# Kernel tuning notes

Measured on AMD Instinct MI355X. Metric: run time of the kernel, lower is better.

The kernel has to match this reference:

```python
import jax, jax.numpy as jnp
import numpy as np

# dims
B, N, T, D = 32, 207, 12, 128
H, HD, L, FF = 8, 16, 4, 512
PL, OD, IN = 12, 1, 1
SCALE = 1.0 / float(np.sqrt(HD))
NEG = -1e9


def ln(x, g, b, eps=1e-5):
    m = jnp.mean(x, -1, keepdims=True)
    v = jnp.mean((x - m) ** 2, -1, keepdims=True)
    return (x - m) * jax.lax.rsqrt(v + eps) * g + b


def setup_inputs() -> dict:
    key = jax.random.key(0)
    keys = iter(jax.random.split(key, 48))
    def rn(shape, s=0.02):
        return jax.random.normal(next(keys), shape, jnp.float32) * s
    z = lambda *s: jnp.zeros(s, jnp.float32)
    o = lambda *s: jnp.ones(s, jnp.float32)
    inp = {
        "x": jax.random.normal(next(keys), (B, N, T, IN), jnp.float32),
        "adj": jax.random.randint(next(keys), (N, N), 0, 2, jnp.int32),
        "Wi": rn((IN, D)), "bi": z(D),
        # spatial blocks (stacked over L layers)
        "Wq": rn((L, D, D)), "Wk": rn((L, D, D)), "Wv": rn((L, D, D)),
        "Wo": rn((L, D, D)), "bo": z(L, D),
        "sW1": rn((L, D, FF)), "sB1": z(L, FF), "sW2": rn((L, FF, D)), "sB2": z(L, D),
        "sg1": o(L, D), "sh1": z(L, D), "sg2": o(L, D), "sh2": z(L, D),
        # temporal blocks
        "Win": rn((L, D, 3 * D)), "Bin": z(L, 3 * D), "Wout": rn((L, D, D)), "Bout": z(L, D),
        "tW1": rn((L, D, FF)), "tB1": z(L, FF), "tW2": rn((L, FF, D)), "tB2": z(L, D),
        "tg1": o(L, D), "th1": z(L, D), "tg2": o(L, D), "th2": z(L, D),
        # prediction head
        "P1": rn((D, 2 * D)), "Pb1": z(2 * D), "P2": rn((2 * D, D)), "Pb2": z(D),
        "P3": rn((D, PL * OD)), "Pb3": z(PL * OD),
    }
    return inp


def reference(x, adj, Wi, bi, Wq, Wk, Wv, Wo, bo, sW1, sB1, sW2, sB2,
              sg1, sh1, sg2, sh2, Win, Bin, Wout, Bout, tW1, tB1, tW2, tB2,
              tg1, th1, tg2, th2, P1, Pb1, P2, Pb2, P3, Pb3):
    mask = (adj == 0)  # [N,N] True = masked (no edge)
    cmask = jnp.triu(jnp.ones((T, T), bool), 1)  # causal mask over time
    h = x @ Wi + bi  # [B,N,T,D]
    for l in range(L):
        # --- spatial adjacency-masked attention (vectorized over t) ---
        xn = ln(h, sg1[l], sh1[l])
        q = (xn @ Wq[l]).reshape(B, N, T, H, HD)
        k = (xn @ Wk[l]).reshape(B, N, T, H, HD)
        v = (xn @ Wv[l]).reshape(B, N, T, H, HD)
        sc = jnp.einsum('bnthd,bmthd->bthnm', q, k) * SCALE  # [B,T,H,N,N]
        sc = jnp.where(mask[None, None, None], NEG, sc)
        a = jax.nn.softmax(sc, -1)
        o = jnp.einsum('bthnm,bmthd->bnthd', a, v).reshape(B, N, T, D)
        h = h + o @ Wo[l] + bo[l]
        xn = ln(h, sg2[l], sh2[l])
        h = h + jax.nn.relu(xn @ sW1[l] + sB1[l]) @ sW2[l] + sB2[l]
        # --- temporal causal attention (per node) ---
        xn = ln(h, tg1[l], th1[l])
        qkv = xn @ Win[l] + Bin[l]
        q, k, v = jnp.split(qkv, 3, -1)
        q = q.reshape(B, N, T, H, HD)
        k = k.reshape(B, N, T, H, HD)
        v = v.reshape(B, N, T, H, HD)
        sc = jnp.einsum('bnthd,bnshd->bnhts', q, k) * SCALE  # [B,N,H,T,T]
        sc = jnp.where(cmask[None, None, None], NEG, sc)
        a = jax.nn.softmax(sc, -1)
        o = jnp.einsum('bnhts,bnshd->bnthd', a, v).reshape(B, N, T, D)
        h = h + o @ Wout[l] + Bout[l]
        xn = ln(h, tg2[l], th2[l])
        h = h + jax.nn.relu(xn @ tW1[l] + tB1[l]) @ tW2[l] + tB2[l]
    # prediction head on last time step
    hl = h[:, :, -1, :]  # [B,N,D]
    zz = jax.nn.relu(hl @ P1 + Pb1)
    zz = jax.nn.relu(zz @ P2 + Pb2)
    return (zz @ P3 + Pb3).reshape(B, N, PL, OD)
```

## Files before the change

### kernel.cpp

```cpp
#include <hip/hip_runtime.h>
#include <hip/hip_bf16.h>

#define B_   32
#define N_   207
#define T_   12
#define D_   128
#define H_   8
#define HD_  16
#define L_   4
#define FF_  512
#define PL_  12
#define TOK  (B_*N_*T_)
#define ROWS2 (B_*N_)
#define SCALE_ 0.25f
#define NEG_  -1e9f
#define NPAD 208
#define KQ2  24
#define KVH  232
#define SLAB 3312

typedef __hip_bfloat16 bf16;
typedef unsigned int u32;
typedef __attribute__((ext_vector_type(8))) short bf16x8;
typedef __attribute__((ext_vector_type(8))) _Float16 f16x8;
typedef __attribute__((ext_vector_type(4))) float f32x4;

__device__ __forceinline__ float b2f(bf16 x){ return __bfloat162float(x); }
__device__ __forceinline__ bf16  f2b(float x){ return __float2bfloat16(x); }

__device__ __forceinline__ void gll16(const bf16* g, bf16* l){
  __builtin_amdgcn_global_load_lds((const __attribute__((address_space(1))) void*)g,
                                   (__attribute__((address_space(3))) void*)l, 16, 0, 0);
}

__global__ void detect_k(const void* x, int* flag){
  __shared__ int cnt[256];
  const unsigned short* u = (const unsigned short*)x;
  int ok = 0;
  for (int i = threadIdx.x; i < 4096; i += 256){
    unsigned int bits = ((unsigned int)u[i]) << 16;
    float f = __uint_as_float(bits);
    float a = fabsf(f);
    if (f == 0.0f || (a > 1e-4f && a < 64.0f)) ok++;
  }
  cnt[threadIdx.x] = ok;
  __syncthreads();
  for (int s = 128; s > 0; s >>= 1){
    if (threadIdx.x < s) cnt[threadIdx.x] += cnt[threadIdx.x + s];
    __syncthreads();
  }
  if (threadIdx.x == 0) *flag = (cnt[0] > 3686) ? 1 : 0;
}

struct FlatArgs {
  const void* src[24];
  long long dst[24];
  int cum[25];
};
__global__ void cvt_flat_k(FlatArgs a, bf16* base, const int* flag, int total){
  int i = blockIdx.x*256 + threadIdx.x;
  if (i >= total) return;
  int j = 0;
  while (i >= a.cum[j+1]) j++;
  int loc = i - a.cum[j];
  float v = (*flag) ? b2f(((const bf16*)a.src[j])[loc]) : ((const float*)a.src[j])[loc];
  base[a.dst[j] + loc] = f2b(v);
}

struct TArgs {
  const void* src[10];
  long long dst[10];
  int K[10], Nc[10], Lstr[10], ro[10];
  float scale[10];
  int cum[11];
};
__global__ void cvt_t_k(TArgs a, bf16* base, const int* flag, int total){
  int i = blockIdx.x*256 + threadIdx.x;
  if (i >= total) return;
  int j = 0;
  while (i >= a.cum[j+1]) j++;
  int loc = i - a.cum[j];
  int KN = a.K[j]*a.Nc[j];
  int l = loc / KN; int rm = loc - l*KN; int k = rm / a.Nc[j]; int n = rm - k*a.Nc[j];
  float v = (*flag) ? b2f(((const bf16*)a.src[j])[loc]) : ((const float*)a.src[j])[loc];
  base[a.dst[j] + (long long)l*a.Lstr[j] + (long long)(a.ro[j]+n)*a.K[j] + k] = f2b(v*a.scale[j]);
}

__global__ void abits_k(const int* adj, u32* out){
  int i = blockIdx.x*256 + threadIdx.x;
  if (i >= NPAD*7) return;
  int n = i / 7, wj = i % 7;
  u32 v = 0;
  if (n < N_){
    for (int bit = 0; bit < 32; bit++){
      int m = wj*32 + bit;
      if (m < N_ && adj[n*N_ + m] != 0) v |= (1u << bit);
    }
  }
  out[i] = v;
}

__global__ void embed_ln_k(const bf16* x, const bf16* Wi, const bf16* bi,
                           const bf16* g, const bf16* bta, float* h, bf16* xnb){
  int wave = threadIdx.x >> 6, lane = threadIdx.x & 63;
  int tok = blockIdx.x*4 + wave;
  if (tok >= TOK) return;
  float xv = b2f(x[tok]);
  float v0 = xv*b2f(Wi[lane])    + b2f(bi[lane]);
  float v1 = xv*b2f(Wi[lane+64]) + b2f(bi[lane+64]);
  float* hp = h + (size_t)tok*D_;
  hp[lane] = v0; hp[lane+64] = v1;
  float s = v0 + v1;
  for (int off = 32; off >= 1; off >>= 1) s += __shfl_xor(s, off, 64);
  float m = s * (1.0f/128.0f);
  float d0 = v0 - m, d1 = v1 - m;
  float vv = d0*d0 + d1*d1;
  for (int off = 32; off >= 1; off >>= 1) vv += __shfl_xor(vv, off, 64);
  float r = rsqrtf(vv*(1.0f/128.0f) + 1e-5f);
  bf16* op = xnb + (size_t)tok*D_;
  op[lane]    = f2b(d0*r*b2f(g[lane])    + b2f(bta[lane]));
  op[lane+64] = f2b(d1*r*b2f(g[lane+64]) + b2f(bta[lane+64]));
}

__global__ __launch_bounds__(256) void mgemm_k(const bf16* __restrict__ A,
    const bf16* __restrict__ Wt, const bf16* __restrict__ bias,
    bf16* __restrict__ outp, int ldo, int Ktot, int relu){
  __shared__ __align__(16) bf16 As[128*32];
  __shared__ __align__(16) bf16 Bs[128*32];
  int tid = threadIdx.x;
  int rowBase = blockIdx.y * 128, colBase = blockIdx.x * 128;
  int w = tid >> 6, lane = tid & 63, quad = lane >> 4, cl = lane & 15;
  int waveM = w >> 1, waveN = w & 1;
  f32x4 accr[4][4];
  #pragma unroll
  for (int i = 0; i < 4; i++)
    #pragma unroll
    for (int j = 0; j < 4; j++) accr[i][j] = (f32x4){0.f,0.f,0.f,0.f};
  int lr = tid >> 2, kc = tid & 3;
  const bf16* Ap = A  + (size_t)(rowBase + lr)*Ktot + kc*8;
  const bf16* Bp = Wt + (size_t)(colBase + lr)*Ktot + kc*8;
  bf16* AsW = As + tid*8;
  bf16* BsW = Bs + tid*8;
  for (int kk = 0; kk < Ktot; kk += 32){
    __syncthreads();
    gll16(Ap + kk, AsW);
    gll16(Ap + (size_t)64*Ktot + kk, AsW + 64*32);
    gll16(Bp + kk, BsW);
    gll16(Bp + (size_t)64*Ktot + kk, BsW + 64*32);
    __syncthreads();
    bf16x8 af[4], bfr[4];
    #pragma unroll
    for (int mi = 0; mi < 4; mi++)
      af[mi] = *(const bf16x8*)(As + (waveM*64 + mi*16 + cl)*32 + quad*8);
    #pragma unroll
    for (int nj = 0; nj < 4; nj++)
      bfr[nj] = *(const bf16x8*)(Bs + (waveN*64 + nj*16 + cl)*32 + quad*8);
    #pragma unroll
    for (int mi = 0; mi < 4; mi++)
      #pragma unroll
      for (int nj = 0; nj < 4; nj++)
        accr[mi][nj] = __builtin_amdgcn_mfma_f32_16x16x32_bf16(af[mi], bfr[nj], accr[mi][nj], 0,0,0);
  }
  float bv[4];
  #pragma unroll
  for (int nj = 0; nj < 4; nj++)
    bv[nj] = bias ? b2f(bias[colBase + waveN*64 + nj*16 + cl]) : 0.0f;
  #pragma unroll
  for (int mi = 0; mi < 4; mi++){
    int row0 = rowBase + waveM*64 + mi*16 + quad*4;
    #pragma unroll
    for (int nj = 0; nj < 4; nj++){
      int col = colBase + waveN*64 + nj*16 + cl;
      #pragma unroll
      for (int r = 0; r < 4; r++){
        float v = accr[mi][nj][r] + bv[nj];
        if (relu) v = fmaxf(v, 0.0f);
        outp[(size_t)(row0+r)*ldo + col] = f2b(v);
      }
    }
  }
}

__global__ __launch_bounds__(256) void mgemm_qkvT_k(const bf16* __restrict__ A,
    const bf16* __restrict__ Wt, bf16* __restrict__ sQ,
    bf16* __restrict__ sK, bf16* __restrict__ sV){
  __shared__ __align__(16) bf16 As[128*32];
  __shared__ __align__(16) bf16 Bs[128*32];
  const int Ktot = 128;
  int tid = threadIdx.x;
  int rowBase = blockIdx.y * 128, colBase = blockIdx.x * 128;
  int w = tid >> 6, lane = tid & 63, quad = lane >> 4, cl = lane & 15;
  int waveM = w >> 1, waveN = w & 1;
  f32x4 accr[4][4];
  #pragma unroll
  for (int i = 0; i < 4; i++)
    #pragma unroll
    for (int j = 0; j < 4; j++) accr[i][j] = (f32x4){0.f,0.f,0.f,0.f};
  int lr = tid >> 2, kc = tid & 3;
  const bf16* Ap = A  + (size_t)(rowBase + lr)*Ktot + kc*8;
  const bf16* Bp = Wt + (size_t)(colBase + lr)*Ktot + kc*8;
  bf16* AsW = As + tid*8;
  bf16* BsW = Bs + tid*8;
  for (int kk = 0; kk < Ktot; kk += 32){
    __syncthreads();
    gll16(Ap + kk, AsW);
    gll16(Ap + (size_t)64*Ktot + kk, AsW + 64*32);
    gll16(Bp + kk, BsW);
    gll16(Bp + (size_t)64*Ktot + kk, BsW + 64*32);
    __syncthreads();
    bf16x8 af[4], bfr[4];
    #pragma unroll
    for (int mi = 0; mi < 4; mi++)
      af[mi] = *(const bf16x8*)(As + (waveM*64 + mi*16 + cl)*32 + quad*8);
    #pragma unroll
    for (int nj = 0; nj < 4; nj++)
      bfr[nj] = *(const bf16x8*)(Bs + (waveN*64 + nj*16 + cl)*32 + quad*8);
    #pragma unroll
    for (int mi = 0; mi < 4; mi++)
      #pragma unroll
      for (int nj = 0; nj < 4; nj++)
        accr[mi][nj] = __builtin_amdgcn_mfma_f32_16x16x32_bf16(af[mi], bfr[nj], accr[mi][nj], 0,0,0);
  }
  #pragma unroll
  for (int mi = 0; mi < 4; mi++){
    #pragma unroll
    for (int r = 0; r < 4; r++){
      int tok = rowBase + waveM*64 + mi*16 + quad*4 + r;
      int bn = tok / T_; int t = tok - bn*T_;
      int b = bn / N_;  int n = bn - b*N_;
      size_t base = ((size_t)(b*T_ + t)*H_)*SLAB + n*16 + cl;
      #pragma unroll
      for (int nj = 0; nj < 4; nj++){
        int col = colBase + waveN*64 + nj*16;
        int part = col >> 7, hh = (col >> 4) & 7;
        bf16* dst = (part == 0) ? sQ : (part == 1) ? sK : sV;
        dst[base + (size_t)hh*SLAB] = f2b(accr[mi][nj][r]);
      }
    }
  }
}

__global__ __launch_bounds__(256) void mgemm_ln_k(const bf16* __restrict__ A,
    const bf16* __restrict__ Wt, const bf16* __restrict__ bias,
    float* __restrict__ hout, int Ktot,
    const bf16* __restrict__ g, const bf16* __restrict__ bta,
    bf16* __restrict__ xnb){
  __shared__ __align__(16) bf16 As[128*32];
  __shared__ __align__(16) bf16 Bs[128*32];
  __shared__ float red[2][128][2];
  int tid = threadIdx.x;
  int rowBase = blockIdx.y * 128;
  int w = tid >> 6, lane = tid & 63, quad = lane >> 4, cl = lane & 15;
  int waveM = w >> 1, waveN = w & 1;
  f32x4 accr[4][4];
  #pragma unroll
  for (int i = 0; i < 4; i++)
    #pragma unroll
    for (int j = 0; j < 4; j++) accr[i][j] = (f32x4){0.f,0.f,0.f,0.f};
  int lr = tid >> 2, kc = tid & 3;
  const bf16* Ap = A  + (size_t)(rowBase + lr)*Ktot + kc*8;
  const bf16* Bp = Wt + (size_t)lr*Ktot + kc*8;
  bf16* AsW = As + tid*8;
  bf16* BsW = Bs + tid*8;
  for (int kk = 0; kk < Ktot; kk += 32){
    __syncthreads();
    gll16(Ap + kk, AsW);
    gll16(Ap + (size_t)64*Ktot + kk, AsW + 64*32);
    gll16(Bp + kk, BsW);
    gll16(Bp + (size_t)64*Ktot + kk, BsW + 64*32);
    __syncthreads();
    bf16x8 af[4], bfr[4];
    #pragma unroll
    for (int mi = 0; mi < 4; mi++)
      af[mi] = *(const bf16x8*)(As + (waveM*64 + mi*16 + cl)*32 + quad*8);
    #pragma unroll
    for (int nj = 0; nj < 4; nj++)
      bfr[nj] = *(const bf16x8*)(Bs + (waveN*64 + nj*16 + cl)*32 + quad*8);
    #pragma unroll
    for (int mi = 0; mi < 4; mi++)
      #pragma unroll
      for (int nj = 0; nj < 4; nj++)
        accr[mi][nj] = __builtin_amdgcn_mfma_f32_16x16x32_bf16(af[mi], bfr[nj], accr[mi][nj], 0,0,0);
  }
  int colW = waveN*64;
  float bv[4];
  #pragma unroll
  for (int nj = 0; nj < 4; nj++)
    bv[nj] = bias ? b2f(bias[colW + nj*16 + cl]) : 0.0f;
  float hv[4][4][4];
  float psum[4][4], psq[4][4];
  #pragma unroll
  for (int mi = 0; mi < 4; mi++)
    #pragma unroll
    for (int r = 0; r < 4; r++){ psum[mi][r] = 0.f; psq[mi][r] = 0.f; }
  #pragma unroll
  for (int mi = 0; mi < 4; mi++){
    #pragma unroll
    for (int r = 0; r < 4; r++){
      int row = rowBase + waveM*64 + mi*16 + quad*4 + r;
      #pragma unroll
      for (int nj = 0; nj < 4; nj++){
        int col = colW + nj*16 + cl;
        size_t idx = (size_t)row*D_ + col;
        float v = hout[idx] + accr[mi][nj][r] + bv[nj];
        hout[idx] = v;
        hv[mi][nj][r] = v;
        psum[mi][r] += v; psq[mi][r] += v*v;
      }
    }
  }
  if (g){
    #pragma unroll
    for (int off = 1; off <= 8; off <<= 1)
      #pragma unroll
      for (int mi = 0; mi < 4; mi++)
        #pragma unroll
        for (int r = 0; r < 4; r++){
          psum[mi][r] += __shfl_xor(psum[mi][r], off, 64);
          psq[mi][r]  += __shfl_xor(psq[mi][r],  off, 64);
        }
    if (cl == 0){
      #pragma unroll
      for (int mi = 0; mi < 4; mi++)
        #pragma unroll
        for (int r = 0; r < 4; r++){
          int rl = waveM*64 + mi*16 + quad*4 + r;
          red[waveN][rl][0] = psum[mi][r];
          red[waveN][rl][1] = psq[mi][r];
        }
    }
    __syncthreads();
    float gv[4], btv[4];
    #pragma unroll
    for (int nj = 0; nj < 4; nj++){
      int col = colW + nj*16 + cl;
      gv[nj] = b2f(g[col]); btv[nj] = b2f(bta[col]);
    }
    #pragma unroll
    for (int mi = 0; mi < 4; mi++){
      #pragma unroll
      for (int r = 0; r < 4; r++){
        int rl = waveM*64 + mi*16 + quad*4 + r;
        float s = red[0][rl][0] + red[1][rl][0];
        float q = red[0][rl][1] + red[1][rl][1];
        float mean = s*(1.0f/128.0f);
        float var  = q*(1.0f/128.0f) - mean*mean;
        float rstd = rsqrtf(var + 1e-5f);
        int row = rowBase + rl;
        #pragma unroll
        for (int nj = 0; nj < 4; nj++){
          int col = colW + nj*16 + cl;
          xnb[(size_t)row*D_ + col] = f2b((hv[mi][nj][r]-mean)*rstd*gv[nj] + btv[nj]);
        }
      }
    }
  }
}

__global__ __launch_bounds__(256,3) void sattn_k(const bf16* __restrict__ sQ,
    const bf16* __restrict__ sK, const bf16* __restrict__ sV,
    const u32* __restrict__ abg, bf16* __restrict__ ob){
  __shared__ __align__(16) bf16     Ks[NPAD*KQ2];
  __shared__ __align__(16) _Float16 Vt[16*KVH];
  __shared__ __align__(16) _Float16 Ps[4*16*KVH];
  __shared__ u32 abs_[NPAD*7];
  int tid = threadIdx.x;
  int bid = blockIdx.x;
  int hh = bid & 7; int bt = bid >> 3; int t = bt % T_; int b = bt / T_;
  const bf16* Kslab = sK + (size_t)bid*SLAB;
  const bf16* Vslab = sV + (size_t)bid*SLAB;
  const bf16* Qslab = sQ + (size_t)bid*SLAB;
  for (int i = tid; i < 16*25; i += 256){ int d = i/25, c = 207 + i%25; Vt[d*KVH + c] = (_Float16)0.0f; }
  for (int i = tid; i < 64*24; i += 256){ int row = i/24, c = 208 + i%24; Ps[row*KVH + c] = (_Float16)0.0f; }
  for (int c = tid; c < 414; c += 256){
    bf16x8 kv = *(const bf16x8*)(Kslab + c*8);
    int n = c >> 1, dh = (c & 1)*8;
    *(bf16x8*)(Ks + n*KQ2 + dh) = kv;
  }
  for (int i = tid; i < SLAB; i += 256){
    int n = i >> 4, d = i & 15;
    Vt[d*KVH + n] = (_Float16)b2f(Vslab[i]);
  }
  for (int i = tid; i < NPAD*7; i += 256) abs_[i] = abg[i];
  __syncthreads();

  int lane = tid & 63, w = tid >> 6, quad = lane >> 4, cl = lane & 15;
  int nstripes = (w == 0) ? 4 : 3;
  for (int si = 0; si < nstripes; si++){
    int mi = w + si*4;
    bf16x8 aq = (bf16x8){0,0,0,0,0,0,0,0};
    {
      int n = mi*16 + cl; if (n > N_-1) n = N_-1;
      if (quad < 2) aq = *(const bf16x8*)(Qslab + n*16 + quad*8);
    }
    f32x4 s[13];
    #pragma unroll
    for (int nj = 0; nj < 13; nj++){
      bf16x8 bk = (bf16x8){0,0,0,0,0,0,0,0};
      if (quad < 2) bk = *(const bf16x8*)(Ks + (nj*16 + cl)*KQ2 + quad*8);
      f32x4 z = {0.f,0.f,0.f,0.f};
      s[nj] = __builtin_amdgcn_mfma_f32_16x16x32_bf16(aq, bk, z, 0,0,0);
    }
    int row0 = mi*16 + quad*4;
    _Float16* Pw = Ps + w*16*KVH;
    #pragma unroll
    for (int r = 0; r < 4; r++){
      const u32* ab = abs_ + (row0 + r)*7;
      float mx = -3.4e38f;
      #pragma unroll
      for (int nj = 0; nj < 13; nj++){
        int cg = nj*16 + cl;
        float v = s[nj][r];
        if (nj == 12 && cl == 15) v = -3.4e38f;
        else if (!((ab[cg >> 5] >> (cg & 31)) & 1)) v = NEG_;
        s[nj][r] = v;
        mx = fmaxf(mx, v);
      }
      for (int off = 1; off < 16; off <<= 1) mx = fmaxf(mx, __shfl_xor(mx, off, 64));
      float sum = 0.0f;
      #pragma unroll
      for (int nj = 0; nj < 13; nj++){
        float e = __expf(s[nj][r] - mx);
        s[nj][r] = e; sum += e;
      }
      for (int off = 1; off < 16; off <<= 1) sum += __shfl_xor(sum, off, 64);
      float inv = 1.0f/sum;
      _Float16* Pr = Pw + (quad*4 + r)*KVH;
      #pragma unroll
      for (int nj = 0; nj < 13; nj++) Pr[nj*16 + cl] = (_Float16)(s[nj][r]*inv);
    }
    __threadfence_block();
    f32x4 o = {0.f,0.f,0.f,0.f};
    #pragma unroll
    for (int kt = 0; kt < 7; kt++){
      f16x8 ap = *(const f16x8*)(Pw + cl*KVH + kt*32 + quad*8);
      f16x8 bv = *(const f16x8*)(Vt + cl*KVH + kt*32 + quad*8);
      o = __builtin_amdgcn_mfma_f32_16x16x32_f16(ap, bv, o, 0,0,0);
    }
    #pragma unroll
    for (int r = 0; r < 4; r++){
      int rg = row0 + r;
      if (rg < N_)
        ob[((size_t)((b*N_ + rg)*T_ + t))*D_ + hh*HD_ + cl] = f2b(o[r]);
    }
    __threadfence_block();
  }
}

__global__ void tattn_k(const bf16* qkv, bf16* ob){
  int bid = blockIdx.x; int b = bid / N_, n = bid % N_;
  __shared__ float qs[T_*D_];
  __shared__ float ks[T_*D_];
  __shared__ float vs[T_*D_];
  size_t rowb = ((size_t)(b*N_+n)*T_)*384;
  const u32* src = (const u32*)(qkv + rowb);
  for (int idx = threadIdx.x; idx < T_*192; idx += 128){
    int tt = idx / 192, cw = idx - tt*192;
    u32 pr = src[tt*192 + cw];
    union { u32 u; bf16 b[2]; } cv; cv.u = pr;
    float v0 = b2f(cv.b[0]), v1 = b2f(cv.b[1]);
    int arr = cw >> 6, cp2 = (cw & 63)*2;
    float* dst = (arr == 0) ? qs : (arr == 1) ? ks : vs;
    dst[tt*128 + cp2] = v0; dst[tt*128 + cp2 + 1] = v1;
  }
  __syncthreads();
  int p = threadIdx.x;
  if (p < H_*T_){
    int hh = p / T_, t = p - hh*T_;
    float qreg[16];
    for (int d = 0; d < 16; d++) qreg[d] = qs[t*128 + hh*16 + d];
    float sc[12]; float mx = -3.4e38f;
    for (int s = 0; s < 12; s++){
      float a = 0.0f;
      for (int d = 0; d < 16; d++) a += qreg[d]*ks[s*128 + hh*16 + d];
      a = (s <= t) ? a*SCALE_ : -3.4e38f;
      sc[s] = a; mx = fmaxf(mx, a);
    }
    float ssum = 0.0f;
    for (int s = 0; s < 12; s++){
      float e = (s <= t) ? __expf(sc[s]-mx) : 0.0f;
      sc[s] = e; ssum += e;
    }
    float inv = 1.0f/ssum;
    size_t obase = ((size_t)(b*N_+n)*T_ + t)*D_ + hh*16;
    for (int d = 0; d < 16; d++){
      float acc = 0.0f;
      for (int s = 0; s < 12; s++) acc += sc[s]*vs[s*128 + hh*16 + d];
      ob[obase + d] = f2b(acc*inv);
    }
  }
}

__global__ void gemm_k(const bf16* A, int lda, const bf16* W, const bf16* bias,
                       void* outp, int ldo, int M, int Ncols, int K, int relu, int acc){
  __shared__ float Ast[16*68];
  __shared__ float Ws [16*68];
  int tx = threadIdx.x & 15, ty = threadIdx.x >> 4;
  int rowBase = blockIdx.y * 64, colBase = blockIdx.x * 64;
  float accr[4][4];
  for (int i = 0; i < 4; i++) for (int j = 0; j < 4; j++) accr[i][j] = 0.0f;
  for (int kk = 0; kk < K; kk += 16){
    int kq = threadIdx.x & 15, r0 = threadIdx.x >> 4;
    for (int it = 0; it < 4; it++){
      int r = r0 + it*16, row = rowBase + r;
      float v = 0.0f;
      if (row < M) v = b2f(A[(size_t)row*lda + kk + kq]);
      Ast[kq*68 + r] = v;
    }
    int c = threadIdx.x & 63, w0 = threadIdx.x >> 6;
    for (int it = 0; it < 4; it++){
      int kr = w0 + it*4;
      Ws[kr*68 + c] = b2f(W[(size_t)(kk+kr)*Ncols + colBase + c]);
    }
    __syncthreads();
    for (int k = 0; k < 16; k++){
      float av[4], wv[4];
      for (int i = 0; i < 4; i++) av[i] = Ast[k*68 + ty*4 + i];
      for (int j = 0; j < 4; j++) wv[j] = Ws[k*68 + tx*4 + j];
      for (int i = 0; i < 4; i++)
        for (int j = 0; j < 4; j++) accr[i][j] += av[i]*wv[j];
    }
    __syncthreads();
  }
  for (int i = 0; i < 4; i++){
    int row = rowBase + ty*4 + i;
    if (row >= M) continue;
    for (int j = 0; j < 4; j++){
      int col = colBase + tx*4 + j;
      float v = accr[i][j];
      if (bias) v += b2f(bias[col]);
      if (relu) v = fmaxf(v, 0.0f);
      if (acc) ((float*)outp)[(size_t)row*ldo + col] += v;
      else     ((bf16*)outp)[(size_t)row*ldo + col] = f2b(v);
    }
  }
}

__global__ void gather_k(const float* h, bf16* hlb){
  int i = blockIdx.x*256 + threadIdx.x;
  if (i >= ROWS2*D_) return;
  int r = i >> 7, d = i & 127;
  hlb[i] = f2b(h[((size_t)r*T_ + (T_-1))*D_ + d]);
}

__global__ void head3_k(const bf16* z2, const bf16* P3, const bf16* Pb3,
                        void* out, int out_n, const int* flag){
  int i = blockIdx.x*256 + threadIdx.x;
  if (i >= out_n) return;
  int r = i / PL_, j = i - r*PL_;
  float acc = b2f(Pb3[j]);
  for (int d = 0; d < 128; d++) acc += b2f(z2[(size_t)r*128 + d]) * b2f(P3[d*PL_ + j]);
  if (*flag) ((bf16*)out)[i] = f2b(acc);
  else       ((float*)out)[i] = acc;
}

extern "C" void kernel_launch(void* const* d_in, const int* in_sizes, int n_in,
                              void* d_out, int out_size, void* d_ws, size_t ws_size,
                              hipStream_t stream){
  size_t HB = (size_t)TOK*D_*4;
  size_t XB = (size_t)TOK*D_*2;
  size_t RB = (size_t)TOK*D_*8;
  float* h    = (float*)d_ws;
  bf16*  xnb  = (bf16*)((char*)d_ws + HB);
  bf16*  reg_ = (bf16*)((char*)d_ws + HB + XB);
  bf16*  cvt  = (bf16*)((char*)d_ws + HB + XB + RB);
  bf16*  wsb  = (bf16*)d_ws;
  const int FIDX[34] = {0,2,3,4,5,6,7,8,9,10,11,12,13,14,15,16,17,18,19,20,
                        21,22,23,24,25,26,27,28,29,30,31,32,33,34};
  bf16* cp[34];
  size_t off = 0;
  for (int i = 0; i < 34; i++){ cp[i] = cvt + off; off += (size_t)in_sizes[FIDX[i]]; }
  char* tail   = (char*)d_ws + HB + XB + RB + ((off*2 + 255) & ~(size_t)255);
  u32*  abg    = (u32*)tail;
  bf16* qkvw   = (bf16*)(tail + 8192);
  int*  flag   = (int*)(tail + 8192 + (size_t)L_*384*128*2);

  const bf16 *x_c=cp[0], *Wi_c=cp[1], *bi_c=cp[2],
             *Wo_t=cp[6], *bo_c=cp[7], *sW1_t=cp[8], *sB1_c=cp[9], *sW2_t=cp[10], *sB2_c=cp[11],
             *sg1_c=cp[12], *sh1_c=cp[13], *sg2_c=cp[14], *sh2_c=cp[15], *Win_t=cp[16], *Bin_c=cp[17],
             *Wout_t=cp[18], *Bout_c=cp[19], *tW1_t=cp[20], *tB1_c=cp[21], *tW2_t=cp[22], *tB2_c=cp[23],
             *tg1_c=cp[24], *th1_c=cp[25], *tg2_c=cp[26], *th2_c=cp[27], *P1_c=cp[28], *Pb1_c=cp[29],
             *P2_c=cp[30], *Pb2_c=cp[31], *P3_c=cp[32], *Pb3_c=cp[33];
  const int* adj = (const int*)d_in[1];

  bf16* sQ   = reg_;
  bf16* sK   = reg_ + (size_t)TOK*128;
  bf16* sV   = reg_ + (size_t)2*TOK*128;
  bf16* ob   = reg_ + (size_t)3*TOK*128;
  bf16* qkvb = reg_;
  bf16* ffb  = reg_;

  detect_k<<<1, 256, 0, stream>>>(d_in[0], flag);

  {
    const int FLAT[24] = {0,1,2,7,9,11,12,13,14,15,17,19,21,23,24,25,26,27,28,29,30,31,32,33};
    FlatArgs fa; int c = 0;
    for (int ii = 0; ii < 24; ii++){
      int ci = FLAT[ii];
      fa.src[ii] = d_in[FIDX[ci]];
      fa.dst[ii] = (long long)(cp[ci] - wsb);
      fa.cum[ii] = c;
      c += in_sizes[FIDX[ci]];
    }
    fa.cum[24] = c;
    cvt_flat_k<<<(c+255)/256, 256, 0, stream>>>(fa, wsb, flag, c);
  }
  {
    TArgs ta; int c = 0;
    const void* srcs[10] = {d_in[4], d_in[5], d_in[6], d_in[7], d_in[9], d_in[11],
                            d_in[17], d_in[19], d_in[21], d_in[23]};
    bf16* dsts[10] = {qkvw, qkvw, qkvw, cp[6], cp[8], cp[10], cp[16], cp[18], cp[20], cp[22]};
    int Ks_[10]   = {128,128,128, 128, 128, 512, 128, 128, 128, 512};
    int Ncs[10]   = {128,128,128, 128, 512, 128, 384, 128, 512, 128};
    int Lst[10]   = {384*128,384*128,384*128, 128*128, 128*512, 512*128, 128*384, 128*128, 128*512, 512*128};
    int ros[10]   = {0,128,256, 0,0,0, 0,0,0, 0};
    for (int j = 0; j < 10; j++){
      ta.src[j] = srcs[j];
      ta.dst[j] = (long long)(dsts[j] - wsb);
      ta.K[j] = Ks_[j]; ta.Nc[j] = Ncs[j]; ta.Lstr[j] = Lst[j]; ta.ro[j] = ros[j];
      ta.scale[j] = (j == 0) ? SCALE_ : 1.0f;
      ta.cum[j] = c;
      c += L_*Ks_[j]*Ncs[j];
    }
    ta.cum[10] = c;
    cvt_t_k<<<(c+255)/256, 256, 0, stream>>>(ta, wsb, flag, c);
  }
  abits_k<<<(NPAD*7+255)/256, 256, 0, stream>>>(adj, abg);
  embed_ln_k<<<TOK/4, 256, 0, stream>>>(x_c, Wi_c, bi_c, sg1_c, sh1_c, h, xnb);

  const dim3 gP  (1, TOK/128);
  const dim3 gF1 (4, TOK/128);
  const dim3 gQKV(3, TOK/128);

  for (int l = 0; l < L_; l++){
    mgemm_qkvT_k<<<gQKV, 256, 0, stream>>>(xnb, qkvw + (size_t)l*384*128, sQ, sK, sV);
    sattn_k<<<B_*T_*H_, 256, 0, stream>>>(sQ, sK, sV, abg, ob);
    mgemm_ln_k<<<gP, 256, 0, stream>>>(ob, Wo_t + (size_t)l*D_*D_, bo_c + l*D_, h, D_,
                                       sg2_c + l*D_, sh2_c + l*D_, xnb);
    mgemm_k<<<gF1, 256, 0, stream>>>(xnb, sW1_t + (size_t)l*D_*FF_, sB1_c + l*FF_, ffb, FF_, D_, 1);
    mgemm_ln_k<<<gP, 256, 0, stream>>>(ffb, sW2_t + (size_t)l*FF_*D_, sB2_c + l*D_, h, FF_,
                                       tg1_c + l*D_, th1_c + l*D_, xnb);
    mgemm_k<<<gQKV, 256, 0, stream>>>(xnb, Win_t + (size_t)l*D_*384, Bin_c + l*384, qkvb, 384, D_, 0);
    tattn_k<<<B_*N_, 128, 0, stream>>>(qkvb, ob);
    mgemm_ln_k<<<gP, 256, 0, stream>>>(ob, Wout_t + (size_t)l*D_*D_, Bout_c + l*D_, h, D_,
                                       tg2_c + l*D_, th2_c + l*D_, xnb);
    mgemm_k<<<gF1, 256, 0, stream>>>(xnb, tW1_t + (size_t)l*D_*FF_, tB1_c + l*FF_, ffb, FF_, D_, 1);
    const bf16* gnext = (l < L_-1) ? (sg1_c + (l+1)*D_) : nullptr;
    const bf16* bnext = (l < L_-1) ? (sh1_c + (l+1)*D_) : nullptr;
    mgemm_ln_k<<<gP, 256, 0, stream>>>(ffb, tW2_t + (size_t)l*FF_*D_, tB2_c + l*D_, h, FF_,
                                       gnext, bnext, xnb);
  }

  bf16* hlb = reg_;
  bf16* z1  = reg_ + (size_t)ROWS2*128;
  bf16* z2  = z1   + (size_t)ROWS2*256;
  gather_k<<<(ROWS2*D_)/256, 256, 0, stream>>>(h, hlb);
  gemm_k<<<dim3(256/64, (ROWS2+63)/64), 256, 0, stream>>>(hlb, 128, P1_c, Pb1_c, z1, 256, ROWS2, 256, 128, 1, 0);
  gemm_k<<<dim3(128/64, (ROWS2+63)/64), 256, 0, stream>>>(z1, 256, P2_c, Pb2_c, z2, 128, ROWS2, 128, 256, 1, 0);
  head3_k<<<(out_size+255)/256, 256, 0, stream>>>(z2, P3_c, Pb3_c, d_out, out_size, flag);
}
```

Before: 1.751 ms.

## Precompute additive spatial mask in MFMA layout and drop softmax max pass

```diff
diff --git a/kernel.cpp b/kernel.cpp
--- a/kernel.cpp
+++ b/kernel.cpp
@@ -18,6 +18,7 @@
 #define KQ2  24
 #define KVH  232
 #define SLAB 3312
+#define MSK_N (13*13*256)
 
 typedef __hip_bfloat16 bf16;
 typedef unsigned int u32;
@@ -86,18 +87,20 @@
   base[a.dst[j] + (long long)l*a.Lstr[j] + (long long)(a.ro[j]+n)*a.K[j] + k] = f2b(v*a.scale[j]);
 }
 
-__global__ void abits_k(const int* adj, u32* out){
+__global__ void maskc_k(const int* adj, float* maskg){
   int i = blockIdx.x*256 + threadIdx.x;
-  if (i >= NPAD*7) return;
-  int n = i / 7, wj = i % 7;
-  u32 v = 0;
-  if (n < N_){
-    for (int bit = 0; bit < 32; bit++){
-      int m = wj*32 + bit;
-      if (m < N_ && adj[n*N_ + m] != 0) v |= (1u << bit);
-    }
-  }
-  out[i] = v;
+  if (i >= MSK_N) return;
+  int cell = i >> 8;
+  int mi = cell / 13, nj = cell - mi*13;
+  int rem = i & 255;
+  int lane = rem >> 2, r = rem & 3;
+  int quad = lane >> 4, cl = lane & 15;
+  int row = mi*16 + quad*4 + r; if (row > 206) row = 206;
+  int col = nj*16 + cl;
+  float v;
+  if (col > 206) v = -1e30f;
+  else v = adj[row*N_ + col] ? 0.0f : NEG_;
+  maskg[i] = v;
 }
 
 __global__ void embed_ln_k(const bf16* x, const bf16* Wi, const bf16* bi,
@@ -359,11 +362,10 @@
 
 __global__ __launch_bounds__(256,3) void sattn_k(const bf16* __restrict__ sQ,
     const bf16* __restrict__ sK, const bf16* __restrict__ sV,
-    const u32* __restrict__ abg, bf16* __restrict__ ob){
+    const float* __restrict__ maskg, bf16* __restrict__ ob){
   __shared__ __align__(16) bf16     Ks[NPAD*KQ2];
   __shared__ __align__(16) _Float16 Vt[16*KVH];
   __shared__ __align__(16) _Float16 Ps[4*16*KVH];
-  __shared__ u32 abs_[NPAD*7];
   int tid = threadIdx.x;
   int bid = blockIdx.x;
   int hh = bid & 7; int bt = bid >> 3; int t = bt % T_; int b = bt / T_;
@@ -381,7 +383,6 @@
     int n = i >> 4, d = i & 15;
     Vt[d*KVH + n] = (_Float16)b2f(Vslab[i]);
   }
-  for (int i = tid; i < NPAD*7; i += 256) abs_[i] = abg[i];
   __syncthreads();
 
   int lane = tid & 63, w = tid >> 6, quad = lane >> 4, cl = lane & 15;
@@ -393,41 +394,31 @@
       int n = mi*16 + cl; if (n > N_-1) n = N_-1;
       if (quad < 2) aq = *(const bf16x8*)(Qslab + n*16 + quad*8);
     }
+    const float* mrow = maskg + ((size_t)mi*13)*256 + lane*4;
     f32x4 s[13];
     #pragma unroll
     for (int nj = 0; nj < 13; nj++){
       bf16x8 bk = (bf16x8){0,0,0,0,0,0,0,0};
       if (quad < 2) bk = *(const bf16x8*)(Ks + (nj*16 + cl)*KQ2 + quad*8);
-      f32x4 z = {0.f,0.f,0.f,0.f};
-      s[nj] = __builtin_amdgcn_mfma_f32_16x16x32_bf16(aq, bk, z, 0,0,0);
+      f32x4 c0 = *(const f32x4*)(mrow + nj*256);
+      s[nj] = __builtin_amdgcn_mfma_f32_16x16x32_bf16(aq, bk, c0, 0,0,0);
     }
     int row0 = mi*16 + quad*4;
     _Float16* Pw = Ps + w*16*KVH;
+    float invr[4];
     #pragma unroll
     for (int r = 0; r < 4; r++){
-      const u32* ab = abs_ + (row0 + r)*7;
-      float mx = -3.4e38f;
+      float sum = 0.0f;
       #pragma unroll
       for (int nj = 0; nj < 13; nj++){
-        int cg = nj*16 + cl;
-        float v = s[nj][r];
-        if (nj == 12 && cl == 15) v = -3.4e38f;
-        else if (!((ab[cg >> 5] >> (cg & 31)) & 1)) v = NEG_;
-        s[nj][r] = v;
-        mx = fmaxf(mx, v);
-      }
-      for (int off = 1; off < 16; off <<= 1) mx = fmaxf(mx, __shfl_xor(mx, off, 64));
-      float sum = 0.0f;
-      #pragma unroll
-      for (int nj = 0; nj < 13; nj++){
-        float e = __expf(s[nj][r] - mx);
+        float e = __expf(s[nj][r]);
         s[nj][r] = e; sum += e;
       }
       for (int off = 1; off < 16; off <<= 1) sum += __shfl_xor(sum, off, 64);
-      float inv = 1.0f/sum;
+      invr[r] = 1.0f/sum;
       _Float16* Pr = Pw + (quad*4 + r)*KVH;
       #pragma unroll
-      for (int nj = 0; nj < 13; nj++) Pr[nj*16 + cl] = (_Float16)(s[nj][r]*inv);
+      for (int nj = 0; nj < 13; nj++) Pr[nj*16 + cl] = (_Float16)s[nj][r];
     }
     __threadfence_block();
     f32x4 o = {0.f,0.f,0.f,0.f};
@@ -441,7 +432,7 @@
     for (int r = 0; r < 4; r++){
       int rg = row0 + r;
       if (rg < N_)
-        ob[((size_t)((b*N_ + rg)*T_ + t))*D_ + hh*HD_ + cl] = f2b(o[r]);
+        ob[((size_t)((b*N_ + rg)*T_ + t))*D_ + hh*HD_ + cl] = f2b(o[r]*invr[r]);
     }
     __threadfence_block();
   }
@@ -571,9 +562,9 @@
   size_t off = 0;
   for (int i = 0; i < 34; i++){ cp[i] = cvt + off; off += (size_t)in_sizes[FIDX[i]]; }
   char* tail   = (char*)d_ws + HB + XB + RB + ((off*2 + 255) & ~(size_t)255);
-  u32*  abg    = (u32*)tail;
-  bf16* qkvw   = (bf16*)(tail + 8192);
-  int*  flag   = (int*)(tail + 8192 + (size_t)L_*384*128*2);
+  float* maskg = (float*)tail;
+  bf16* qkvw   = (bf16*)(tail + (size_t)MSK_N*4);
+  int*  flag   = (int*)(tail + (size_t)MSK_N*4 + (size_t)L_*384*128*2);
 
   const bf16 *x_c=cp[0], *Wi_c=cp[1], *bi_c=cp[2],
              *Wo_t=cp[6], *bo_c=cp[7], *sW1_t=cp[8], *sB1_c=cp[9], *sW2_t=cp[10], *sB2_c=cp[11],
@@ -625,7 +616,7 @@
     ta.cum[10] = c;
     cvt_t_k<<<(c+255)/256, 256, 0, stream>>>(ta, wsb, flag, c);
   }
-  abits_k<<<(NPAD*7+255)/256, 256, 0, stream>>>(adj, abg);
+  maskc_k<<<(MSK_N+255)/256, 256, 0, stream>>>(adj, maskg);
   embed_ln_k<<<TOK/4, 256, 0, stream>>>(x_c, Wi_c, bi_c, sg1_c, sh1_c, h, xnb);
 
   const dim3 gP  (1, TOK/128);
@@ -634,7 +625,7 @@
 
   for (int l = 0; l < L_; l++){
     mgemm_qkvT_k<<<gQKV, 256, 0, stream>>>(xnb, qkvw + (size_t)l*384*128, sQ, sK, sV);
-    sattn_k<<<B_*T_*H_, 256, 0, stream>>>(sQ, sK, sV, abg, ob);
+    sattn_k<<<B_*T_*H_, 256, 0, stream>>>(sQ, sK, sV, maskg, ob);
     mgemm_ln_k<<<gP, 256, 0, stream>>>(ob, Wo_t + (size_t)l*D_*D_, bo_c + l*D_, h, D_,
                                        sg2_c + l*D_, sh2_c + l*D_, xnb);
     mgemm_k<<<gF1, 256, 0, stream>>>(xnb, sW1_t + (size_t)l*D_*FF_, sB1_c + l*FF_, ffb, FF_, D_, 1);
```

Measured after the change: 1.732 ms. About the same (-1.1%).
